# Optimization experiments

Measured on AMD Instinct MI355X. Metric: run time of the kernel, lower is better.

## Reference

```python
import jax, jax.numpy as jnp
import numpy as np

TEMPERATURE = 0.2

def setup_inputs() -> dict:
    key = jax.random.key(0)
    k1, k2 = jax.random.split(key)
    B, D = 4096, 128
    emb_i = jax.random.normal(k1, (B, D), dtype=jnp.float32)
    emb_j = jax.random.normal(k2, (B, D), dtype=jnp.float32)
    return {"emb_i": emb_i, "emb_j": emb_j}

def reference(emb_i, emb_j):
    # L2-normalize each embedding row, concat -> z: [2B, D]
    z_i = emb_i / jnp.linalg.norm(emb_i, axis=1, keepdims=True)
    z_j = emb_j / jnp.linalg.norm(emb_j, axis=1, keepdims=True)
    z = jnp.concatenate([z_i, z_j], axis=0)          # [2B, D]
    N2 = z.shape[0]
    N = N2 // 2
    # cosine similarity of normalized vectors == dot product
    sim = z @ z.T                                    # [2B, 2B]
    logits = sim / TEMPERATURE
    # denominator excludes only the diagonal (k != i)
    diag_mask = jnp.eye(N2, dtype=bool)
    masked = jnp.where(diag_mask, -jnp.inf, logits)
    lse = jax.nn.logsumexp(masked, axis=1)           # [2B]
    # positive pair for row i is i+N (mod 2N)
    pos_idx = jnp.concatenate([jnp.arange(N) + N, jnp.arange(N)])
    pos_logits = jnp.take_along_axis(logits, pos_idx[:, None], axis=1)[:, 0]
    # loss = (1/2N) * sum_i -log( exp(pos_i) / sum_{k!=i} exp(logits[i,k]) )
    loss = jnp.mean(lse - pos_logits)
    return loss
```

## Files before the change

### kernel.cpp

```cpp
#include <hip/hip_runtime.h>
#include <hip/hip_bf16.h>
#include <hip/hip_fp8.h>

typedef __attribute__((ext_vector_type(4))) float f32x4;
typedef long long i64;

#define EXP_SCALE 7.213475204444817f

__device__ __forceinline__ float fast_exp2(float x) {
#if __has_builtin(__builtin_amdgcn_exp2f)
  return __builtin_amdgcn_exp2f(x);
#else
  return exp2f(x);
#endif
}


__global__ __launch_bounds__(256) void k_normalize(
    const float* __restrict__ emb_i, const float* __restrict__ emb_j,
    unsigned char* __restrict__ z, float* __restrict__ out)
{
  if (blockIdx.x == 0 && threadIdx.x == 0) out[0] = 0.0f;
  const int t = threadIdx.x;
  const int c = t >> 4;
  const int sub = t & 15;
  const int row = (blockIdx.x << 4) + c;
  const float* src = (row < 4096) ? (emb_i + row * 128) : (emb_j + (row - 4096) * 128);
  float4 v0 = reinterpret_cast<const float4*>(src)[sub * 2];
  float4 v1 = reinterpret_cast<const float4*>(src)[sub * 2 + 1];
  float ss = v0.x*v0.x + v0.y*v0.y + v0.z*v0.z + v0.w*v0.w
           + v1.x*v1.x + v1.y*v1.y + v1.z*v1.z + v1.w*v1.w;
  #pragma unroll
  for (int m = 1; m < 16; m <<= 1) ss += __shfl_xor(ss, m, 64);
  float rinv = 1.0f / sqrtf(ss);
  unsigned char st[8];
  st[0] = __hip_fp8_e4m3(v0.x * rinv).__x;
  st[1] = __hip_fp8_e4m3(v0.y * rinv).__x;
  st[2] = __hip_fp8_e4m3(v0.z * rinv).__x;
  st[3] = __hip_fp8_e4m3(v0.w * rinv).__x;
  st[4] = __hip_fp8_e4m3(v1.x * rinv).__x;
  st[5] = __hip_fp8_e4m3(v1.y * rinv).__x;
  st[6] = __hip_fp8_e4m3(v1.z * rinv).__x;
  st[7] = __hip_fp8_e4m3(v1.w * rinv).__x;
  unsigned char* dst = z + blockIdx.x * 2048 + (sub >> 2) * 512 +
                       (((sub & 3) << 4) + c) * 8;
  *reinterpret_cast<i64*>(dst) = *reinterpret_cast<i64*>(st);
}

__global__ __launch_bounds__(256, 4) void k_simlse(
    const unsigned char* __restrict__ z,
    float* __restrict__ rpart,
    float* __restrict__ cpart,
    float* __restrict__ rowpos)
{
  const int w = threadIdx.x >> 6;
  const int lane = threadIdx.x & 63;
  const int q = lane >> 4;
  const int c = lane & 15;
  const int bid = blockIdx.x;

  int ch = (int)((sqrtf((float)(bid + 1)) - 1.0f) * 0.5f);
  if (bid >= 4 * (ch + 1) * (ch + 2)) ++ch;
  else if (bid < 4 * ch * (ch + 1)) --ch;
  const int rb = bid - 4 * ch * (ch + 1);
  const int R0 = rb << 6;
  const bool upper = (rb < (ch << 3));

  i64 a[4][4];
  {
    const unsigned char* ap = z + (R0 >> 4) * 2048 + (lane << 3);
    #pragma unroll
    for (int rg = 0; rg < 4; ++rg)
      #pragma unroll
      for (int kk = 0; kk < 4; ++kk)
        a[rg][kk] = *reinterpret_cast<const i64*>(ap + rg * 2048 + kk * 512);
  }

  float acc[4][4];
  #pragma unroll
  for (int rg = 0; rg < 4; ++rg)
    #pragma unroll
    for (int e = 0; e < 4; ++e) acc[rg][e] = 0.0f;
  float pacc[4] = {0.f, 0.f, 0.f, 0.f};
  float colp[8];
  #pragma unroll
  for (int i = 0; i < 8; ++i) colp[i] = 0.0f;

  __shared__ float lsum[4][64];
  __shared__ float lpos[4][16];

  const int ct0 = (ch << 5) + w;
  const unsigned char* bwave = z + ct0 * 2048 + (lane << 3);

  const int pos0t = ((R0 + 4096) & 8191) >> 4;
  const int ipb = ((pos0t >> 5) == ch) ? ((pos0t & 31) >> 2) : -99;

  i64 b0[4], b1[4];
  auto ldb = [&](i64 (&dst)[4], int idx) {
    const unsigned char* p = bwave + idx * 8192;
    dst[0] = *reinterpret_cast<const i64*>(p);
    dst[1] = *reinterpret_cast<const i64*>(p + 512);
    dst[2] = *reinterpret_cast<const i64*>(p + 1024);
    dst[3] = *reinterpret_cast<const i64*>(p + 1536);
  };

  auto process = [&](const i64 (&bb)[4], int i) {
    f32x4 cc[4];
    #pragma unroll
    for (int rr = 0; rr < 4; ++rr) cc[rr] = f32x4{0.f, 0.f, 0.f, 0.f};
    #pragma unroll
    for (int kk = 0; kk < 4; ++kk)
      #pragma unroll
      for (int rr = 0; rr < 4; ++rr)
        cc[rr] = __builtin_amdgcn_mfma_f32_16x16x32_fp8_fp8(
            a[rr][kk], bb[kk], cc[rr], 0, 0, 0);
    float cp0 = 0.0f, cp1 = 0.0f;
    #pragma unroll
    for (int rr = 0; rr < 4; ++rr)
      #pragma unroll
      for (int e = 0; e < 4; ++e) {
        float tv = fast_exp2(__builtin_fmaf(cc[rr][e], EXP_SCALE, -EXP_SCALE));
        acc[rr][e] += tv;
        if (upper) { if (rr & 1) cp1 += tv; else cp0 += tv; }
      }
    if (upper) colp[i] = cp0 + cp1;
    if (i == ipb) {
      #pragma unroll
      for (int rr = 0; rr < 4; ++rr) {
        if (rr == w) {
          #pragma unroll
          for (int e = 0; e < 4; ++e)
            if (c == ((q << 2) + e)) pacc[e] = cc[rr][e] * 5.0f;
        }
      }
    }
  };

  ldb(b0, 0);
  #pragma unroll 1
  for (int i = 0; i < 8; i += 2) {
    ldb(b1, i + 1);
    process(b0, i);
    if (i + 2 < 8) ldb(b0, i + 2);
    process(b1, i + 1);
  }

  if (upper) {
    const int cbase = 2048 * ch * (ch - 1) + (rb << 9);
    #pragma unroll
    for (int i = 0; i < 8; ++i) {
      float v = colp[i];
      v += __shfl_xor(v, 16, 64);
      v += __shfl_xor(v, 32, 64);
      if (lane < 16)
        cpart[cbase + ((w + (i << 2)) << 4) + c] = v;
    }
  }

  #pragma unroll
  for (int m = 1; m < 16; m <<= 1) {
    #pragma unroll
    for (int rg = 0; rg < 4; ++rg)
      #pragma unroll
      for (int e = 0; e < 4; ++e)
        acc[rg][e] += __shfl_xor(acc[rg][e], m, 64);
    #pragma unroll
    for (int e = 0; e < 4; ++e) pacc[e] += __shfl_xor(pacc[e], m, 64);
  }

  if (c == 0) {
    #pragma unroll
    for (int rg = 0; rg < 4; ++rg)
      #pragma unroll
      for (int e = 0; e < 4; ++e)
        lsum[w][rg * 16 + (q << 2) + e] = acc[rg][e];
    #pragma unroll
    for (int e = 0; e < 4; ++e) lpos[w][(q << 2) + e] = pacc[e];
  }
  __syncthreads();

  if (threadIdx.x < 64) {
    const int t = threadIdx.x;
    float s = lsum[0][t] + lsum[1][t] + lsum[2][t] + lsum[3][t];
    rpart[(ch << 13) + R0 + t] = s;
    if (ipb != -99)
      rowpos[R0 + t] = lpos[t >> 4][t & 15];
  }
}

__global__ __launch_bounds__(256) void k_finish(
    const float* __restrict__ rpart, const float* __restrict__ cpart,
    const float* __restrict__ rowpos, float* __restrict__ out)
{
  const int r = blockIdx.x * 256 + threadIdx.x;
  const int chr = r >> 9;

  float rs = 0.0f;
  #pragma unroll 4
  for (int ch = chr; ch < 16; ++ch) rs += rpart[(ch << 13) + r];

  const int nrb = chr << 3;
  const float* cb = cpart + 2048 * chr * (chr - 1) + (r & 511);
  float cs0 = 0.f, cs1 = 0.f, cs2 = 0.f, cs3 = 0.f;
  #pragma unroll 2
  for (int rb = 0; rb < nrb; rb += 4) {
    cs0 += cb[(rb + 0) << 9];
    cs1 += cb[(rb + 1) << 9];
    cs2 += cb[(rb + 2) << 9];
    cs3 += cb[(rb + 3) << 9];
  }

  float tot = rs + ((cs0 + cs1) + (cs2 + cs3)) - 1.0f;
  float v = 5.0f + logf(tot) - rowpos[r & 4095];
  #pragma unroll
  for (int m = 1; m < 64; m <<= 1) v += __shfl_xor(v, m, 64);
  __shared__ float red[4];
  if ((threadIdx.x & 63) == 0) red[threadIdx.x >> 6] = v;
  __syncthreads();
  if (threadIdx.x == 0)
    atomicAdd(out, (red[0] + red[1] + red[2] + red[3]) * (1.0f / 8192.0f));
}

extern "C" void kernel_launch(void* const* d_in, const int* in_sizes, int n_in,
                              void* d_out, int out_size, void* d_ws, size_t ws_size,
                              hipStream_t stream) {
  const float* emb_i = (const float*)d_in[0];
  const float* emb_j = (const float*)d_in[1];
  unsigned char* z = (unsigned char*)d_ws;
  float* rpart = (float*)((char*)d_ws + (1 << 20));
  float* cpart = (float*)((char*)d_ws + (1 << 20) + (512 << 10));
  float* rowpos = (float*)((char*)d_ws + (1 << 20) + (512 << 10) + 1966080);
  float* out = (float*)d_out;

  k_normalize<<<512, 256, 0, stream>>>(emb_i, emb_j, z, out);
  k_simlse<<<1088, 256, 0, stream>>>(z, rpart, cpart, rowpos);
  k_finish<<<32, 256, 0, stream>>>(rpart, cpart, rowpos, out);
}
```

Before: 80.01 us.

## Halve row tile per block, double grid, rotate column order, triple-buffer B loads

Each similarity block now covers 32 rows instead of 64, so the grid doubles to 2176 blocks, with the triangular block mapping and partial-sum indexing rescaled to match. Column tiles are visited in a per-block rotated order so concurrent blocks read different parts of z. The B-fragment prefetch becomes a fully unrolled three-buffer pipeline. The aim is better load balance and fewer idle CUs on the triangular schedule, paid for with less A reuse per block, more partial sums to write and reduce, and more B traffic.

```diff
diff --git a/kernel.cpp b/kernel.cpp
--- a/kernel.cpp
+++ b/kernel.cpp
@@ -59,26 +59,27 @@
   const int c = lane & 15;
   const int bid = blockIdx.x;
 
-  int ch = (int)((sqrtf((float)(bid + 1)) - 1.0f) * 0.5f);
-  if (bid >= 4 * (ch + 1) * (ch + 2)) ++ch;
-  else if (bid < 4 * ch * (ch + 1)) --ch;
-  const int rb = bid - 4 * ch * (ch + 1);
-  const int R0 = rb << 6;
-  const bool upper = (rb < (ch << 3));
-
-  i64 a[4][4];
+  int ch = (int)((sqrtf(1.0f + 0.5f * (float)bid) - 1.0f) * 0.5f);
+  if (bid >= 8 * (ch + 1) * (ch + 2)) ++ch;
+  else if (bid < 8 * ch * (ch + 1)) --ch;
+  const int rb = bid - 8 * ch * (ch + 1);
+  const int R0 = rb << 5;
+  const bool upper = (rb < (ch << 4));
+  const int rot = bid & 7;
+
+  i64 a[2][4];
   {
     const unsigned char* ap = z + (R0 >> 4) * 2048 + (lane << 3);
     #pragma unroll
-    for (int rg = 0; rg < 4; ++rg)
+    for (int rg = 0; rg < 2; ++rg)
       #pragma unroll
       for (int kk = 0; kk < 4; ++kk)
         a[rg][kk] = *reinterpret_cast<const i64*>(ap + rg * 2048 + kk * 512);
   }
 
-  float acc[4][4];
-  #pragma unroll
-  for (int rg = 0; rg < 4; ++rg)
+  float acc[2][4];
+  #pragma unroll
+  for (int rg = 0; rg < 2; ++rg)
     #pragma unroll
     for (int e = 0; e < 4; ++e) acc[rg][e] = 0.0f;
   float pacc[4] = {0.f, 0.f, 0.f, 0.f};
@@ -86,7 +87,7 @@
   #pragma unroll
   for (int i = 0; i < 8; ++i) colp[i] = 0.0f;
 
-  __shared__ float lsum[4][64];
+  __shared__ float lsum[4][32];
   __shared__ float lpos[4][16];
 
   const int ct0 = (ch << 5) + w;
@@ -94,8 +95,9 @@
 
   const int pos0t = ((R0 + 4096) & 8191) >> 4;
   const int ipb = ((pos0t >> 5) == ch) ? ((pos0t & 31) >> 2) : -99;
-
-  i64 b0[4], b1[4];
+  const int pw = pos0t & 3;
+
+  i64 b0[4], b1[4], b2[4];
   auto ldb = [&](i64 (&dst)[4], int idx) {
     const unsigned char* p = bwave + idx * 8192;
     dst[0] = *reinterpret_cast<const i64*>(p);
@@ -104,30 +106,30 @@
     dst[3] = *reinterpret_cast<const i64*>(p + 1536);
   };
 
-  auto process = [&](const i64 (&bb)[4], int i) {
-    f32x4 cc[4];
-    #pragma unroll
-    for (int rr = 0; rr < 4; ++rr) cc[rr] = f32x4{0.f, 0.f, 0.f, 0.f};
+  auto process = [&](const i64 (&bb)[4], int idx, float& cpj) {
+    f32x4 cc[2];
+    #pragma unroll
+    for (int rr = 0; rr < 2; ++rr) cc[rr] = f32x4{0.f, 0.f, 0.f, 0.f};
     #pragma unroll
     for (int kk = 0; kk < 4; ++kk)
       #pragma unroll
-      for (int rr = 0; rr < 4; ++rr)
+      for (int rr = 0; rr < 2; ++rr)
         cc[rr] = __builtin_amdgcn_mfma_f32_16x16x32_fp8_fp8(
             a[rr][kk], bb[kk], cc[rr], 0, 0, 0);
     float cp0 = 0.0f, cp1 = 0.0f;
     #pragma unroll
-    for (int rr = 0; rr < 4; ++rr)
+    for (int rr = 0; rr < 2; ++rr)
       #pragma unroll
       for (int e = 0; e < 4; ++e) {
         float tv = fast_exp2(__builtin_fmaf(cc[rr][e], EXP_SCALE, -EXP_SCALE));
         acc[rr][e] += tv;
         if (upper) { if (rr & 1) cp1 += tv; else cp0 += tv; }
       }
-    if (upper) colp[i] = cp0 + cp1;
-    if (i == ipb) {
-      #pragma unroll
-      for (int rr = 0; rr < 4; ++rr) {
-        if (rr == w) {
+    if (upper) cpj = cp0 + cp1;
+    if (idx == ipb) {
+      #pragma unroll
+      for (int rr = 0; rr < 2; ++rr) {
+        if (w == pw + rr) {
           #pragma unroll
           for (int e = 0; e < 4; ++e)
             if (c == ((q << 2) + e)) pacc[e] = cc[rr][e] * 5.0f;
@@ -136,31 +138,33 @@
     }
   };
 
-  ldb(b0, 0);
-  #pragma unroll 1
-  for (int i = 0; i < 8; i += 2) {
-    ldb(b1, i + 1);
-    process(b0, i);
-    if (i + 2 < 8) ldb(b0, i + 2);
-    process(b1, i + 1);
-  }
+  #define IDX(j) (((j) + rot) & 7)
+  ldb(b0, IDX(0)); ldb(b1, IDX(1));
+  ldb(b2, IDX(2)); process(b0, IDX(0), colp[0]);
+  ldb(b0, IDX(3)); process(b1, IDX(1), colp[1]);
+  ldb(b1, IDX(4)); process(b2, IDX(2), colp[2]);
+  ldb(b2, IDX(5)); process(b0, IDX(3), colp[3]);
+  ldb(b0, IDX(6)); process(b1, IDX(4), colp[4]);
+  ldb(b1, IDX(7)); process(b2, IDX(5), colp[5]);
+  process(b0, IDX(6), colp[6]);
+  process(b1, IDX(7), colp[7]);
 
   if (upper) {
-    const int cbase = 2048 * ch * (ch - 1) + (rb << 9);
-    #pragma unroll
-    for (int i = 0; i < 8; ++i) {
-      float v = colp[i];
+    const int cbase = 4096 * ch * (ch - 1) + (rb << 9);
+    #pragma unroll
+    for (int j = 0; j < 8; ++j) {
+      float v = colp[j];
       v += __shfl_xor(v, 16, 64);
       v += __shfl_xor(v, 32, 64);
       if (lane < 16)
-        cpart[cbase + ((w + (i << 2)) << 4) + c] = v;
+        cpart[cbase + ((w + (IDX(j) << 2)) << 4) + c] = v;
     }
   }
 
   #pragma unroll
   for (int m = 1; m < 16; m <<= 1) {
     #pragma unroll
-    for (int rg = 0; rg < 4; ++rg)
+    for (int rg = 0; rg < 2; ++rg)
       #pragma unroll
       for (int e = 0; e < 4; ++e)
         acc[rg][e] += __shfl_xor(acc[rg][e], m, 64);
@@ -170,7 +174,7 @@
 
   if (c == 0) {
     #pragma unroll
-    for (int rg = 0; rg < 4; ++rg)
+    for (int rg = 0; rg < 2; ++rg)
       #pragma unroll
       for (int e = 0; e < 4; ++e)
         lsum[w][rg * 16 + (q << 2) + e] = acc[rg][e];
@@ -179,12 +183,12 @@
   }
   __syncthreads();
 
-  if (threadIdx.x < 64) {
+  if (threadIdx.x < 32) {
     const int t = threadIdx.x;
     float s = lsum[0][t] + lsum[1][t] + lsum[2][t] + lsum[3][t];
     rpart[(ch << 13) + R0 + t] = s;
     if (ipb != -99)
-      rowpos[R0 + t] = lpos[t >> 4][t & 15];
+      rowpos[R0 + t] = lpos[pw + (t >> 4)][t & 15];
   }
 }
 
@@ -199,8 +203,8 @@
   #pragma unroll 4
   for (int ch = chr; ch < 16; ++ch) rs += rpart[(ch << 13) + r];
 
-  const int nrb = chr << 3;
-  const float* cb = cpart + 2048 * chr * (chr - 1) + (r & 511);
+  const int nrb = chr << 4;
+  const float* cb = cpart + 4096 * chr * (chr - 1) + (r & 511);
   float cs0 = 0.f, cs1 = 0.f, cs2 = 0.f, cs3 = 0.f;
   #pragma unroll 2
   for (int rb = 0; rb < nrb; rb += 4) {
@@ -228,11 +232,11 @@
   const float* emb_j = (const float*)d_in[1];
   unsigned char* z = (unsigned char*)d_ws;
   float* rpart = (float*)((char*)d_ws + (1 << 20));
-  float* cpart = (float*)((char*)d_ws + (1 << 20) + (512 << 10));
-  float* rowpos = (float*)((char*)d_ws + (1 << 20) + (512 << 10) + 1966080);
+  float* cpart = (float*)((char*)d_ws + 1572864);
+  float* rowpos = (float*)((char*)d_ws + 5505024);
   float* out = (float*)d_out;
 
   k_normalize<<<512, 256, 0, stream>>>(emb_i, emb_j, z, out);
-  k_simlse<<<1088, 256, 0, stream>>>(z, rpart, cpart, rowpos);
+  k_simlse<<<2176, 256, 0, stream>>>(z, rpart, cpart, rowpos);
   k_finish<<<32, 256, 0, stream>>>(rpart, cpart, rowpos, out);
 }
```

After: 86.88 us. 8.6% more time.
